# Kernel tuning notes

Hardware: AMD Instinct MI355X
Metric: run time of the kernel (lower is better)

## Reference

```python
import jax, jax.numpy as jnp
import numpy as np

B, S, V, E, H, C = 64, 256, 50000, 512, 512, 20


def _lstm_dir(x, w_ih, w_hh, b_ih, b_hh):
    # x: [B,S,E]; PyTorch gate order i,f,g,o; returns hidden seq [B,S,H]
    h_dim = w_hh.shape[1]
    xproj = jnp.einsum('bse,ge->bsg', x, w_ih) + b_ih  # [B,S,4H]
    h0 = jnp.zeros((x.shape[0], h_dim), x.dtype)

    def step(carry, xt):
        h, c = carry
        g = xt + h @ w_hh.T + b_hh
        i, f, gg, o = jnp.split(g, 4, axis=-1)
        c = jax.nn.sigmoid(f) * c + jax.nn.sigmoid(i) * jnp.tanh(gg)
        h = jax.nn.sigmoid(o) * jnp.tanh(c)
        return (h, c), h

    _, hs = jax.lax.scan(step, (h0, h0), jnp.swapaxes(xproj, 0, 1))
    return jnp.swapaxes(hs, 0, 1)  # [B,S,H]


def setup_inputs() -> dict:
    key = jax.random.key(0)
    ks = jax.random.split(key, 16)
    sc = lambda fan: 1.0 / np.sqrt(fan)
    return {
        'x': jax.random.randint(ks[0], (B, S), 0, V),
        'embed': jax.random.normal(ks[1], (V, E), jnp.float32),
        'w_ih_f': jax.random.normal(ks[2], (4 * H, E), jnp.float32) * sc(E),
        'w_hh_f': jax.random.normal(ks[3], (4 * H, H), jnp.float32) * sc(H),
        'b_ih_f': jax.random.normal(ks[4], (4 * H,), jnp.float32) * sc(H),
        'b_hh_f': jax.random.normal(ks[5], (4 * H,), jnp.float32) * sc(H),
        'w_ih_b': jax.random.normal(ks[6], (4 * H, E), jnp.float32) * sc(E),
        'w_hh_b': jax.random.normal(ks[7], (4 * H, H), jnp.float32) * sc(H),
        'b_ih_b': jax.random.normal(ks[8], (4 * H,), jnp.float32) * sc(H),
        'b_hh_b': jax.random.normal(ks[9], (4 * H,), jnp.float32) * sc(H),
        'myw': jax.random.normal(ks[10], (2 * H, 1), jnp.float32),
        'lin1_w': jax.random.normal(ks[11], (H, 2 * H), jnp.float32) * sc(2 * H),
        'lin1_b': jax.random.normal(ks[12], (H,), jnp.float32) * sc(2 * H),
        'lin2_w': jax.random.normal(ks[13], (C, H), jnp.float32) * sc(H),
        'lin2_b': jax.random.normal(ks[14], (C,), jnp.float32) * sc(H),
    }


def reference(x, embed, w_ih_f, w_hh_f, b_ih_f, b_hh_f,
              w_ih_b, w_hh_b, b_ih_b, b_hh_b,
              myw, lin1_w, lin1_b, lin2_w, lin2_b):
    emb = embed[x]                                   # [B,S,E] (dropout=eval no-op)
    h_f = _lstm_dir(emb, w_ih_f, w_hh_f, b_ih_f, b_hh_f)
    h_b = _lstm_dir(emb[:, ::-1], w_ih_b, w_hh_b, b_ih_b, b_hh_b)[:, ::-1]
    out = jnp.concatenate([h_f, h_b], axis=-1)       # [B,S,2H]
    # additive-ish attention: weights = exp(tanh(h . w)), normalized by row sum
    p = jnp.exp(jnp.tanh(jnp.einsum('bsd,d->bs', out, myw[:, 0])))  # [B,S]
    denom = jax.lax.stop_gradient(p.sum(axis=1, keepdims=True))     # .data in torch
    pooled = jnp.einsum('bs,bsd->bd', p / denom, out)               # [B,2H]
    h1 = pooled @ lin1_w.T + lin1_b
    return h1 @ lin2_w.T + lin2_b                     # [B,C]
```

## Files before the change

kernel.cpp:

```cpp
#include <hip/hip_runtime.h>

typedef _Float16 f16;
typedef _Float16 half8 __attribute__((ext_vector_type(8)));
typedef float floatx4 __attribute__((ext_vector_type(4)));
typedef unsigned long long u64;
typedef unsigned int u32;
typedef unsigned int u32v4 __attribute__((ext_vector_type(4)));

#define NB 64
#define NS 256
#define NE 512
#define NH 512
#define NG 2048
#define NN 4096

#define HB_B 40
#define HB_KT 320

#define OFF_XP     0
#define OFF_EMB    134217728
#define OFF_WCAT   150994944
#define OFF_WHH    155189248
#define OFF_HSEQ   159383552
#define OFF_BIAS   193200128
#define OFF_HEXT   OFF_EMB

__device__ __forceinline__ void cbar() {
  asm volatile("" ::: "memory");
}
__device__ __forceinline__ float fast_tanh(float x) {
  float e = __expf(2.f * x);
  return 1.f - 2.f / (1.f + e);
}
__device__ __forceinline__ u64 sysld(const u64* p) {
  return __hip_atomic_load(p, __ATOMIC_RELAXED, __HIP_MEMORY_SCOPE_SYSTEM);
}
__device__ __forceinline__ void glds16(const void* g, void* l) {
  __builtin_amdgcn_global_load_lds(
      (const __attribute__((address_space(1))) void*)g,
      (__attribute__((address_space(3))) void*)(__typeof__((__attribute__((address_space(3))) void*)0))(unsigned long)(l),
      16, 0, 0);
}

__global__ void k_prep(float* bias,
                       const float* bihf, const float* bhhf,
                       const float* bihb, const float* bhhb) {
  int id = blockIdx.x * 256 + threadIdx.x;
  bias[id] = (id < 2048) ? (bihf[id] + bhhf[id]) : (bihb[id - 2048] + bhhb[id - 2048]);
}

__global__ void k_zero(uint4* p) {
  uint4 z; z.x = 0; z.y = 0; z.z = 0; z.w = 0;
  p[blockIdx.x * 256 + threadIdx.x] = z;
}

__global__ void k_embed(const int* __restrict__ x, const float* __restrict__ embed,
                        f16* __restrict__ emb_h) {
  int gid = blockIdx.x * 256 + threadIdx.x;
  size_t base = (size_t)gid * 8;
  int r = (int)(base >> 9);
  int e = (int)(base & 511);
  int xi = x[r];
  const float4* src = (const float4*)(embed + (size_t)xi * 512 + e);
  float4 a = src[0], b = src[1];
  half8 h;
  h[0] = (f16)a.x; h[1] = (f16)a.y; h[2] = (f16)a.z; h[3] = (f16)a.w;
  h[4] = (f16)b.x; h[5] = (f16)b.y; h[6] = (f16)b.z; h[7] = (f16)b.w;
  *(half8*)(emb_h + base) = h;
}

__global__ void k_wcast(const float* __restrict__ wihf, const float* __restrict__ wihb,
                        const float* __restrict__ whhf, const float* __restrict__ whhb,
                        f16* __restrict__ w_cat, f16* __restrict__ whh) {
  int gid = blockIdx.x * 256 + threadIdx.x;
  size_t i8 = (size_t)gid * 8;
  const float* src;
  f16* dst;
  if (i8 < 2097152) {
    size_t n = i8 >> 9, k = i8 & 511;
    src = (n < 2048 ? wihf + n * 512 : wihb + (n - 2048) * 512) + k;
    dst = w_cat + i8;
  } else {
    size_t i2 = i8 - 2097152;
    int dir = (int)(i2 >> 20);
    size_t rk = i2 & 1048575;
    src = (dir ? whhb : whhf) + rk;
    dst = whh + i2;
  }
  float4 a = *(const float4*)src, b = *(const float4*)(src + 4);
  half8 h;
  h[0] = (f16)a.x; h[1] = (f16)a.y; h[2] = (f16)a.z; h[3] = (f16)a.w;
  h[4] = (f16)b.x; h[5] = (f16)b.y; h[6] = (f16)b.z; h[7] = (f16)b.w;
  *(half8*)dst = h;
}

__global__ __launch_bounds__(256) void k_gemm(const f16* __restrict__ A,
                                              const f16* __restrict__ Bw,
                                              const float* __restrict__ bias,
                                              f16* __restrict__ xp) {
  __shared__ __align__(16) f16 As[128 * 32];
  __shared__ __align__(16) f16 Bs[128 * 32];
  const int t = threadIdx.x;
  const int m0 = blockIdx.x * 128;
  const int n0 = blockIdx.y * 128;
  const int w = t >> 6, l = t & 63;
  const int wm = w >> 1, wn = w & 1;
  const int l15 = l & 15, q8 = (l >> 4) * 8;

  floatx4 acc[4][4];
#pragma unroll
  for (int mi = 0; mi < 4; mi++)
#pragma unroll
    for (int ni = 0; ni < 4; ni++) {
      acc[mi][ni][0] = 0.f; acc[mi][ni][1] = 0.f;
      acc[mi][ni][2] = 0.f; acc[mi][ni][3] = 0.f;
    }

  for (int kt = 0; kt < 16; kt++) {
#pragma unroll
    for (int i = 0; i < 2; i++) {
      int c = t + 256 * i;
      int row = c >> 2, kc = (c & 3) * 8;
      glds16(A + (size_t)(m0 + row) * 512 + kt * 32 + kc, &As[(64 * w + 256 * i) * 8]);
      glds16(Bw + (size_t)(n0 + row) * 512 + kt * 32 + kc, &Bs[(64 * w + 256 * i) * 8]);
    }
    asm volatile("s_waitcnt vmcnt(0)" ::: "memory");
    __syncthreads();
    half8 af[4], bf[4];
#pragma unroll
    for (int mi = 0; mi < 4; mi++)
      af[mi] = *(const half8*)&As[(wm * 64 + mi * 16 + l15) * 32 + q8];
#pragma unroll
    for (int ni = 0; ni < 4; ni++)
      bf[ni] = *(const half8*)&Bs[(wn * 64 + ni * 16 + l15) * 32 + q8];
#pragma unroll
    for (int mi = 0; mi < 4; mi++)
#pragma unroll
      for (int ni = 0; ni < 4; ni++)
        acc[mi][ni] = __builtin_amdgcn_mfma_f32_16x16x32_f16(af[mi], bf[ni], acc[mi][ni], 0, 0, 0);
    __syncthreads();
  }

#pragma unroll
  for (int ni = 0; ni < 4; ni++) {
    int ng = n0 + wn * 64 + ni * 16 + l15;
    float bv = bias[ng];
#pragma unroll
    for (int mi = 0; mi < 4; mi++) {
      int mg = m0 + wm * 64 + mi * 16 + (l >> 4) * 4;
#pragma unroll
      for (int r = 0; r < 4; r++)
        xp[(size_t)(mg + r) * 4096 + ng] = (f16)(acc[mi][ni][r] + bv);
    }
  }
}

__global__ __launch_bounds__(256) void k_rec(const f16* __restrict__ whh,
                                             const f16* __restrict__ xp,
                                             u32* __restrict__ h_ext,
                                             f16* __restrict__ h_seq) {
  const int blk = blockIdx.x;
  const int dir = blk & 1;
  const int bg  = (blk >> 1) & 7;
  const int jg  = blk >> 4;
  const int t = threadIdx.x;
  const int w = t >> 6, l = t & 63;
  const int l15 = l & 15, q = l >> 4;
  const int lb = l & 7;

  half8 fa[2][16];
  {
#pragma unroll
    for (int mi = 0; mi < 2; mi++) {
      const int gate = 2 * mi + (l15 >> 3);
      const f16* wb = whh + ((size_t)dir * 2048 + gate * 512 + jg * 32 + w * 8 + (l15 & 7)) * 512;
#pragma unroll
      for (int kt = 0; kt < 16; kt++)
        fa[mi][kt] = *(const half8*)(wb + kt * 32 + q * 8);
    }
  }

  __shared__ __align__(16) f16 hbuf[2][16 * HB_KT];
  __shared__ float zw[4][32][18];
  float creg = 0.f;

  const int cb = l >> 3, cu = l & 7;

  const size_t xrow = ((size_t)(8 * bg + lb) * 256);
  const int xc0 = dir * 2048 + (q >> 1) * 512 + jg * 32 + w * 8 + (q & 1) * 4;
  const int xc1 = xc0 + 1024;

  const int slab_rd_base = (dir * 8 + bg) * 4096;
  const int cl_dst0 = (t >> 4) * HB_KT + (t & 3) * 2 * HB_B + ((t >> 2) & 3) * 8;
  const int pub_idx = (jg * 4 + w) * 64 + l;
  const size_t hs_cbase = (size_t)((dir * 16 + jg) * 4 + w) * 256 * 512 + bg * 64 + l;

#pragma unroll 1
  for (int st = 0; st < NS; st++) {
    const int s = dir ? (255 - st) : st;
    const int p = st & 1;

    uint2 xv0 = *(const uint2*)(xp + (xrow + s) * NN + xc0);
    uint2 xv1 = *(const uint2*)(xp + (xrow + s) * NN + xc1);
    cbar();

    {
      const u32* slab32 = h_ext + (p * 16 * 4096) + slab_rd_base;
      const u64* sp = (const u64*)(slab32 + t * 16);
      const u64 tmask = 0xffff0000ffff0000ull;
      const u64 texp = ((u64)(u32)st << 16) | ((u64)(u32)st << 48);
      if (st) __builtin_amdgcn_s_sleep(8);
      while ((sysld(sp + 7) & tmask) != texp) __builtin_amdgcn_s_sleep(1);
      u64 w0, w1, w2, w3, w4, w5, w6, w7;
      while (true) {
        w0 = sysld(sp + 0); w1 = sysld(sp + 1); w2 = sysld(sp + 2); w3 = sysld(sp + 3);
        w4 = sysld(sp + 4); w5 = sysld(sp + 5); w6 = sysld(sp + 6); w7 = sysld(sp + 7);
        u64 ax = w0 & w1 & w2 & w3 & w4 & w5 & w6 & w7;
        u64 ox = w0 | w1 | w2 | w3 | w4 | w5 | w6 | w7;
        if (((ax & tmask) == texp) & ((ox & tmask) == texp)) break;
        __builtin_amdgcn_s_sleep(1);
      }
      u32v4 d0, d1;
      d0[0] = (u32)(w0 & 0xffffu) | ((u32)((w0 >> 32) & 0xffffu) << 16);
      d0[1] = (u32)(w1 & 0xffffu) | ((u32)((w1 >> 32) & 0xffffu) << 16);
      d0[2] = (u32)(w2 & 0xffffu) | ((u32)((w2 >> 32) & 0xffffu) << 16);
      d0[3] = (u32)(w3 & 0xffffu) | ((u32)((w3 >> 32) & 0xffffu) << 16);
      d1[0] = (u32)(w4 & 0xffffu) | ((u32)((w4 >> 32) & 0xffffu) << 16);
      d1[1] = (u32)(w5 & 0xffffu) | ((u32)((w5 >> 32) & 0xffffu) << 16);
      d1[2] = (u32)(w6 & 0xffffu) | ((u32)((w6 >> 32) & 0xffffu) << 16);
      d1[3] = (u32)(w7 & 0xffffu) | ((u32)((w7 >> 32) & 0xffffu) << 16);
      *(u32v4*)&hbuf[p][cl_dst0 + 0]    = d0;
      *(u32v4*)&hbuf[p][cl_dst0 + HB_B] = d1;
    }
    __syncthreads();

    floatx4 a0e, a0o, a1e, a1o;
    a0e[0]=0.f;a0e[1]=0.f;a0e[2]=0.f;a0e[3]=0.f;
    a0o[0]=0.f;a0o[1]=0.f;a0o[2]=0.f;a0o[3]=0.f;
    a1e[0]=0.f;a1e[1]=0.f;a1e[2]=0.f;a1e[3]=0.f;
    a1o[0]=0.f;a1o[1]=0.f;a1o[2]=0.f;a1o[3]=0.f;
#pragma unroll
    for (int kt = 0; kt < 16; kt += 2) {
      half8 bf0 = *(const half8*)&hbuf[p][kt * HB_KT + lb * HB_B + q * 8];
      half8 bf1 = *(const half8*)&hbuf[p][(kt + 1) * HB_KT + lb * HB_B + q * 8];
      a0e = __builtin_amdgcn_mfma_f32_16x16x32_f16(fa[0][kt], bf0, a0e, 0, 0, 0);
      a1e = __builtin_amdgcn_mfma_f32_16x16x32_f16(fa[1][kt], bf0, a1e, 0, 0, 0);
      a0o = __builtin_amdgcn_mfma_f32_16x16x32_f16(fa[0][kt + 1], bf1, a0o, 0, 0, 0);
      a1o = __builtin_amdgcn_mfma_f32_16x16x32_f16(fa[1][kt + 1], bf1, a1o, 0, 0, 0);
    }
    floatx4 acc0 = a0e + a0o;
    floatx4 acc1 = a1e + a1o;

    {
      const f16* x0 = (const f16*)&xv0;
      const f16* x1 = (const f16*)&xv1;
#pragma unroll
      for (int r = 0; r < 4; r++) {
        zw[w][q * 4 + r][l15]      = acc0[r] + (float)x0[r];
        zw[w][16 + q * 4 + r][l15] = acc1[r] + (float)x1[r];
      }
    }
    cbar();
    __builtin_amdgcn_wave_barrier();
    asm volatile("s_waitcnt lgkmcnt(0)" ::: "memory");
    __builtin_amdgcn_sched_barrier(0);

    {
      float iv = zw[w][cu][cb];
      float fv = zw[w][8 + cu][cb];
      float gv = zw[w][16 + cu][cb];
      float ov = zw[w][24 + cu][cb];
      float ig = 1.f / (1.f + __expf(-iv));
      float fg = 1.f / (1.f + __expf(-fv));
      float og = 1.f / (1.f + __expf(-ov));
      creg = fg * creg + ig * fast_tanh(gv);
      f16 hh = (f16)(og * fast_tanh(creg));
      unsigned short hb = __builtin_bit_cast(unsigned short, hh);
      u32 word = (u32)hb | ((u32)(st + 1) << 16);
      u32* wslab = h_ext + (((st + 1) & 1) * 16 * 4096) + slab_rd_base;
      __hip_atomic_store(wslab + pub_idx, word, __ATOMIC_RELAXED,
                         __HIP_MEMORY_SCOPE_SYSTEM);
      h_seq[hs_cbase + (size_t)s * 512] = hh;
    }
  }
}

__global__ __launch_bounds__(256) void k_attn(const f16* __restrict__ h_seq,
                                              const float* __restrict__ myw,
                                              const float* __restrict__ l1w,
                                              const float* __restrict__ l1b,
                                              const float* __restrict__ l2w,
                                              const float* __restrict__ l2b,
                                              float* __restrict__ out) {
  const int b = blockIdx.x;
  const int t = threadIdx.x;
  const int w = t >> 6, l = t & 63;
  float mw[16];
#pragma unroll
  for (int i = 0; i < 16; i += 4) {
    float4 v = *(const float4*)(myw + l * 16 + i);
    mw[i] = v.x; mw[i + 1] = v.y; mw[i + 2] = v.z; mw[i + 3] = v.w;
  }
  float pool[16];
#pragma unroll
  for (int i = 0; i < 16; i++) pool[i] = 0.f;
  float psum = 0.f;

  for (int s = w; s < NS; s += 4) {
    const f16* hp0 = h_seq + ((size_t)(2 * l) * 256 + s) * 512 + b * 8;
    const f16* hp1 = h_seq + ((size_t)(2 * l + 1) * 256 + s) * 512 + b * 8;
    half8 h0 = *(const half8*)hp0;
    half8 h1 = *(const half8*)hp1;
    float hv[16];
#pragma unroll
    for (int i = 0; i < 8; i++) { hv[i] = (float)h0[i]; hv[8 + i] = (float)h1[i]; }
    float d = 0.f;
#pragma unroll
    for (int i = 0; i < 16; i++) d += hv[i] * mw[i];
#pragma unroll
    for (int off = 32; off > 0; off >>= 1) d += __shfl_xor(d, off);
    float p = __expf(tanhf(d));
    psum += p;
#pragma unroll
    for (int i = 0; i < 16; i++) pool[i] += p * hv[i];
  }

  __shared__ float zb[4][1024];
  __shared__ float ps[4];
  __shared__ float pooled[1024];
  __shared__ float h1s[512];
#pragma unroll
  for (int i = 0; i < 16; i++) zb[w][l * 16 + i] = pool[i];
  if (l == 0) ps[w] = psum;
  __syncthreads();
  float denom = ps[0] + ps[1] + ps[2] + ps[3];
  for (int d0 = t; d0 < 1024; d0 += 256)
    pooled[d0] = (zb[0][d0] + zb[1][d0] + zb[2][d0] + zb[3][d0]) / denom;
  __syncthreads();
  for (int r = t; r < 512; r += 256) {
    const float* wr = l1w + (size_t)r * 1024;
    float a = l1b[r];
    for (int k = 0; k < 1024; k += 4) {
      float4 wv = *(const float4*)(wr + k);
      a += wv.x * pooled[k] + wv.y * pooled[k + 1] + wv.z * pooled[k + 2] + wv.w * pooled[k + 3];
    }
    h1s[r] = a;
  }
  __syncthreads();
  if (t < 20) {
    const float* wr = l2w + t * 512;
    float a = l2b[t];
    for (int k = 0; k < 512; k++) a += h1s[k] * wr[k];
    out[b * 20 + t] = a;
  }
}

extern "C" void kernel_launch(void* const* d_in, const int* in_sizes, int n_in,
                              void* d_out, int out_size, void* d_ws, size_t ws_size,
                              hipStream_t stream) {
  (void)in_sizes; (void)n_in; (void)out_size; (void)ws_size;
  const int*   x     = (const int*)d_in[0];
  const float* embed = (const float*)d_in[1];
  const float* wihf  = (const float*)d_in[2];
  const float* whhf  = (const float*)d_in[3];
  const float* bihf  = (const float*)d_in[4];
  const float* bhhf  = (const float*)d_in[5];
  const float* wihb  = (const float*)d_in[6];
  const float* whhb  = (const float*)d_in[7];
  const float* bihb  = (const float*)d_in[8];
  const float* bhhb  = (const float*)d_in[9];
  const float* myw   = (const float*)d_in[10];
  const float* l1w   = (const float*)d_in[11];
  const float* l1b   = (const float*)d_in[12];
  const float* l2w   = (const float*)d_in[13];
  const float* l2b   = (const float*)d_in[14];

  char* ws = (char*)d_ws;
  f16*   xp    = (f16*)(ws + OFF_XP);
  f16*   emb_h = (f16*)(ws + OFF_EMB);
  f16*   w_cat = (f16*)(ws + OFF_WCAT);
  f16*   whh   = (f16*)(ws + OFF_WHH);
  f16*   h_seq = (f16*)(ws + OFF_HSEQ);
  u32*   h_ext = (u32*)(ws + OFF_HEXT);
  float* bias  = (float*)(ws + OFF_BIAS);
  float* out   = (float*)d_out;

  k_prep<<<16, 256, 0, stream>>>(bias, bihf, bhhf, bihb, bhhb);
  k_embed<<<4096, 256, 0, stream>>>(x, embed, emb_h);
  k_wcast<<<2048, 256, 0, stream>>>(wihf, wihb, whhf, whhb, w_cat, whh);
  k_gemm<<<dim3(128, 32), 256, 0, stream>>>(emb_h, w_cat, bias, xp);
  k_zero<<<128, 256, 0, stream>>>((uint4*)(ws + OFF_HEXT));
  k_rec<<<256, 256, 0, stream>>>(whh, xp, h_ext, h_seq);
  k_attn<<<64, 256, 0, stream>>>(h_seq, myw, l1w, l1b, l2w, l2b, out);
}
```

Measured before the change: 1.082 ms.

## Process two batch groups per recurrent block and halve the grid

Each recurrent block now handles two batch groups (bg and bg+4) in turn within every timestep. The register-resident W_hh fragments are reused across both groups, and the launch drops from 256 to 128 blocks. The intent is to cut the number of blocks polling the global handoff slabs and to let one group's work proceed while the other's hidden state is still arriving. The fixed s_sleep before polling is also removed. In exchange, each block does twice the serial work per step, with two block-wide barriers per step, which may lengthen the recurrence critical path.

```diff
diff --git a/kernel.cpp b/kernel.cpp
--- a/kernel.cpp
+++ b/kernel.cpp
@@ -161,8 +161,8 @@
                                              f16* __restrict__ h_seq) {
   const int blk = blockIdx.x;
   const int dir = blk & 1;
-  const int bg  = (blk >> 1) & 7;
-  const int jg  = blk >> 4;
+  const int bgp = (blk >> 1) & 3;
+  const int jg  = blk >> 3;
   const int t = threadIdx.x;
   const int w = t >> 6, l = t & 63;
   const int l15 = l & 15, q = l >> 4;
@@ -180,107 +180,121 @@
     }
   }
 
-  __shared__ __align__(16) f16 hbuf[2][16 * HB_KT];
+  __shared__ __align__(16) f16 hbuf[2][2][16 * HB_KT];
   __shared__ float zw[4][32][18];
-  float creg = 0.f;
+  float creg0 = 0.f, creg1 = 0.f;
 
   const int cb = l >> 3, cu = l & 7;
 
-  const size_t xrow = ((size_t)(8 * bg + lb) * 256);
   const int xc0 = dir * 2048 + (q >> 1) * 512 + jg * 32 + w * 8 + (q & 1) * 4;
   const int xc1 = xc0 + 1024;
 
-  const int slab_rd_base = (dir * 8 + bg) * 4096;
+  const int bgA = bgp, bgB = bgp + 4;
+  const size_t xrowA = ((size_t)(8 * bgA + lb) * 256);
+  const size_t xrowB = ((size_t)(8 * bgB + lb) * 256);
+  const int rdA = (dir * 8 + bgA) * 4096;
+  const int rdB = (dir * 8 + bgB) * 4096;
   const int cl_dst0 = (t >> 4) * HB_KT + (t & 3) * 2 * HB_B + ((t >> 2) & 3) * 8;
   const int pub_idx = (jg * 4 + w) * 64 + l;
-  const size_t hs_cbase = (size_t)((dir * 16 + jg) * 4 + w) * 256 * 512 + bg * 64 + l;
+  const size_t hs_chunk = (size_t)((dir * 16 + jg) * 4 + w) * 256 * 512;
+  const size_t hsA = hs_chunk + bgA * 64 + l;
+  const size_t hsB = hs_chunk + bgB * 64 + l;
+
+  const u64 tmask = 0xffff0000ffff0000ull;
 
 #pragma unroll 1
   for (int st = 0; st < NS; st++) {
     const int s = dir ? (255 - st) : st;
     const int p = st & 1;
-
-    uint2 xv0 = *(const uint2*)(xp + (xrow + s) * NN + xc0);
-    uint2 xv1 = *(const uint2*)(xp + (xrow + s) * NN + xc1);
+    const u64 texp = ((u64)(u32)st << 16) | ((u64)(u32)st << 48);
+
+    uint2 xa0 = *(const uint2*)(xp + (xrowA + s) * NN + xc0);
+    uint2 xa1 = *(const uint2*)(xp + (xrowA + s) * NN + xc1);
+    uint2 xb0 = *(const uint2*)(xp + (xrowB + s) * NN + xc0);
+    uint2 xb1 = *(const uint2*)(xp + (xrowB + s) * NN + xc1);
     cbar();
 
-    {
-      const u32* slab32 = h_ext + (p * 16 * 4096) + slab_rd_base;
-      const u64* sp = (const u64*)(slab32 + t * 16);
-      const u64 tmask = 0xffff0000ffff0000ull;
-      const u64 texp = ((u64)(u32)st << 16) | ((u64)(u32)st << 48);
-      if (st) __builtin_amdgcn_s_sleep(8);
-      while ((sysld(sp + 7) & tmask) != texp) __builtin_amdgcn_s_sleep(1);
-      u64 w0, w1, w2, w3, w4, w5, w6, w7;
-      while (true) {
-        w0 = sysld(sp + 0); w1 = sysld(sp + 1); w2 = sysld(sp + 2); w3 = sysld(sp + 3);
-        w4 = sysld(sp + 4); w5 = sysld(sp + 5); w6 = sysld(sp + 6); w7 = sysld(sp + 7);
-        u64 ax = w0 & w1 & w2 & w3 & w4 & w5 & w6 & w7;
-        u64 ox = w0 | w1 | w2 | w3 | w4 | w5 | w6 | w7;
-        if (((ax & tmask) == texp) & ((ox & tmask) == texp)) break;
-        __builtin_amdgcn_s_sleep(1);
+#pragma unroll
+    for (int c = 0; c < 2; c++) {
+      const int rdb = c ? rdB : rdA;
+      f16* hb = &hbuf[c][p][0];
+
+      {
+        const u32* slab32 = h_ext + (p * 16 * 4096) + rdb;
+        const u64* sp = (const u64*)(slab32 + t * 16);
+        u64 w0, w1, w2, w3, w4, w5, w6, w7;
+        while (true) {
+          w0 = sysld(sp + 0); w1 = sysld(sp + 1); w2 = sysld(sp + 2); w3 = sysld(sp + 3);
+          w4 = sysld(sp + 4); w5 = sysld(sp + 5); w6 = sysld(sp + 6); w7 = sysld(sp + 7);
+          u64 ax = w0 & w1 & w2 & w3 & w4 & w5 & w6 & w7;
+          u64 ox = w0 | w1 | w2 | w3 | w4 | w5 | w6 | w7;
+          if (((ax & tmask) == texp) & ((ox & tmask) == texp)) break;
+          __builtin_amdgcn_s_sleep(1);
+        }
+        u32v4 d0, d1;
+        d0[0] = (u32)(w0 & 0xffffu) | ((u32)((w0 >> 32) & 0xffffu) << 16);
+        d0[1] = (u32)(w1 & 0xffffu) | ((u32)((w1 >> 32) & 0xffffu) << 16);
+        d0[2] = (u32)(w2 & 0xffffu) | ((u32)((w2 >> 32) & 0xffffu) << 16);
+        d0[3] = (u32)(w3 & 0xffffu) | ((u32)((w3 >> 32) & 0xffffu) << 16);
+        d1[0] = (u32)(w4 & 0xffffu) | ((u32)((w4 >> 32) & 0xffffu) << 16);
+        d1[1] = (u32)(w5 & 0xffffu) | ((u32)((w5 >> 32) & 0xffffu) << 16);
+        d1[2] = (u32)(w6 & 0xffffu) | ((u32)((w6 >> 32) & 0xffffu) << 16);
+        d1[3] = (u32)(w7 & 0xffffu) | ((u32)((w7 >> 32) & 0xffffu) << 16);
+        *(u32v4*)&hb[cl_dst0 + 0]    = d0;
+        *(u32v4*)&hb[cl_dst0 + HB_B] = d1;
       }
-      u32v4 d0, d1;
-      d0[0] = (u32)(w0 & 0xffffu) | ((u32)((w0 >> 32) & 0xffffu) << 16);
-      d0[1] = (u32)(w1 & 0xffffu) | ((u32)((w1 >> 32) & 0xffffu) << 16);
-      d0[2] = (u32)(w2 & 0xffffu) | ((u32)((w2 >> 32) & 0xffffu) << 16);
-      d0[3] = (u32)(w3 & 0xffffu) | ((u32)((w3 >> 32) & 0xffffu) << 16);
-      d1[0] = (u32)(w4 & 0xffffu) | ((u32)((w4 >> 32) & 0xffffu) << 16);
-      d1[1] = (u32)(w5 & 0xffffu) | ((u32)((w5 >> 32) & 0xffffu) << 16);
-      d1[2] = (u32)(w6 & 0xffffu) | ((u32)((w6 >> 32) & 0xffffu) << 16);
-      d1[3] = (u32)(w7 & 0xffffu) | ((u32)((w7 >> 32) & 0xffffu) << 16);
-      *(u32v4*)&hbuf[p][cl_dst0 + 0]    = d0;
-      *(u32v4*)&hbuf[p][cl_dst0 + HB_B] = d1;
-    }
-    __syncthreads();
-
-    floatx4 a0e, a0o, a1e, a1o;
-    a0e[0]=0.f;a0e[1]=0.f;a0e[2]=0.f;a0e[3]=0.f;
-    a0o[0]=0.f;a0o[1]=0.f;a0o[2]=0.f;a0o[3]=0.f;
-    a1e[0]=0.f;a1e[1]=0.f;a1e[2]=0.f;a1e[3]=0.f;
-    a1o[0]=0.f;a1o[1]=0.f;a1o[2]=0.f;a1o[3]=0.f;
-#pragma unroll
-    for (int kt = 0; kt < 16; kt += 2) {
-      half8 bf0 = *(const half8*)&hbuf[p][kt * HB_KT + lb * HB_B + q * 8];
-      half8 bf1 = *(const half8*)&hbuf[p][(kt + 1) * HB_KT + lb * HB_B + q * 8];
-      a0e = __builtin_amdgcn_mfma_f32_16x16x32_f16(fa[0][kt], bf0, a0e, 0, 0, 0);
-      a1e = __builtin_amdgcn_mfma_f32_16x16x32_f16(fa[1][kt], bf0, a1e, 0, 0, 0);
-      a0o = __builtin_amdgcn_mfma_f32_16x16x32_f16(fa[0][kt + 1], bf1, a0o, 0, 0, 0);
-      a1o = __builtin_amdgcn_mfma_f32_16x16x32_f16(fa[1][kt + 1], bf1, a1o, 0, 0, 0);
-    }
-    floatx4 acc0 = a0e + a0o;
-    floatx4 acc1 = a1e + a1o;
-
-    {
-      const f16* x0 = (const f16*)&xv0;
-      const f16* x1 = (const f16*)&xv1;
-#pragma unroll
-      for (int r = 0; r < 4; r++) {
-        zw[w][q * 4 + r][l15]      = acc0[r] + (float)x0[r];
-        zw[w][16 + q * 4 + r][l15] = acc1[r] + (float)x1[r];
+      __syncthreads();
+
+      floatx4 a0e, a0o, a1e, a1o;
+      a0e[0]=0.f;a0e[1]=0.f;a0e[2]=0.f;a0e[3]=0.f;
+      a0o[0]=0.f;a0o[1]=0.f;a0o[2]=0.f;a0o[3]=0.f;
+      a1e[0]=0.f;a1e[1]=0.f;a1e[2]=0.f;a1e[3]=0.f;
+      a1o[0]=0.f;a1o[1]=0.f;a1o[2]=0.f;a1o[3]=0.f;
+#pragma unroll
+      for (int kt = 0; kt < 16; kt += 2) {
+        half8 bf0 = *(const half8*)&hb[kt * HB_KT + lb * HB_B + q * 8];
+        half8 bf1 = *(const half8*)&hb[(kt + 1) * HB_KT + lb * HB_B + q * 8];
+        a0e = __builtin_amdgcn_mfma_f32_16x16x32_f16(fa[0][kt], bf0, a0e, 0, 0, 0);
+        a1e = __builtin_amdgcn_mfma_f32_16x16x32_f16(fa[1][kt], bf0, a1e, 0, 0, 0);
+        a0o = __builtin_amdgcn_mfma_f32_16x16x32_f16(fa[0][kt + 1], bf1, a0o, 0, 0, 0);
+        a1o = __builtin_amdgcn_mfma_f32_16x16x32_f16(fa[1][kt + 1], bf1, a1o, 0, 0, 0);
       }
-    }
-    cbar();
-    __builtin_amdgcn_wave_barrier();
-    asm volatile("s_waitcnt lgkmcnt(0)" ::: "memory");
-    __builtin_amdgcn_sched_barrier(0);
-
-    {
-      float iv = zw[w][cu][cb];
-      float fv = zw[w][8 + cu][cb];
-      float gv = zw[w][16 + cu][cb];
-      float ov = zw[w][24 + cu][cb];
-      float ig = 1.f / (1.f + __expf(-iv));
-      float fg = 1.f / (1.f + __expf(-fv));
-      float og = 1.f / (1.f + __expf(-ov));
-      creg = fg * creg + ig * fast_tanh(gv);
-      f16 hh = (f16)(og * fast_tanh(creg));
-      unsigned short hb = __builtin_bit_cast(unsigned short, hh);
-      u32 word = (u32)hb | ((u32)(st + 1) << 16);
-      u32* wslab = h_ext + (((st + 1) & 1) * 16 * 4096) + slab_rd_base;
-      __hip_atomic_store(wslab + pub_idx, word, __ATOMIC_RELAXED,
-                         __HIP_MEMORY_SCOPE_SYSTEM);
-      h_seq[hs_cbase + (size_t)s * 512] = hh;
+      floatx4 acc0 = a0e + a0o;
+      floatx4 acc1 = a1e + a1o;
+
+      {
+        const f16* x0 = (const f16*)(c ? &xb0 : &xa0);
+        const f16* x1 = (const f16*)(c ? &xb1 : &xa1);
+#pragma unroll
+        for (int r = 0; r < 4; r++) {
+          zw[w][q * 4 + r][l15]      = acc0[r] + (float)x0[r];
+          zw[w][16 + q * 4 + r][l15] = acc1[r] + (float)x1[r];
+        }
+      }
+      cbar();
+      __builtin_amdgcn_wave_barrier();
+      asm volatile("s_waitcnt lgkmcnt(0)" ::: "memory");
+      __builtin_amdgcn_sched_barrier(0);
+
+      {
+        float iv = zw[w][cu][cb];
+        float fv = zw[w][8 + cu][cb];
+        float gv = zw[w][16 + cu][cb];
+        float ov = zw[w][24 + cu][cb];
+        float ig = 1.f / (1.f + __expf(-iv));
+        float fg = 1.f / (1.f + __expf(-fv));
+        float og = 1.f / (1.f + __expf(-ov));
+        float cr = c ? creg1 : creg0;
+        cr = fg * cr + ig * fast_tanh(gv);
+        if (c) creg1 = cr; else creg0 = cr;
+        f16 hh = (f16)(og * fast_tanh(cr));
+        unsigned short hb16 = __builtin_bit_cast(unsigned short, hh);
+        u32 word = (u32)hb16 | ((u32)(st + 1) << 16);
+        u32* wslab = h_ext + (((st + 1) & 1) * 16 * 4096) + rdb;
+        __hip_atomic_store(wslab + pub_idx, word, __ATOMIC_RELAXED,
+                           __HIP_MEMORY_SCOPE_SYSTEM);
+        h_seq[(c ? hsB : hsA) + (size_t)s * 512] = hh;
+      }
     }
   }
 }
@@ -390,6 +404,6 @@
   k_wcast<<<2048, 256, 0, stream>>>(wihf, wihb, whhf, whhb, w_cat, whh);
   k_gemm<<<dim3(128, 32), 256, 0, stream>>>(emb_h, w_cat, bias, xp);
   k_zero<<<128, 256, 0, stream>>>((uint4*)(ws + OFF_HEXT));
-  k_rec<<<256, 256, 0, stream>>>(whh, xp, h_ext, h_seq);
+  k_rec<<<128, 256, 0, stream>>>(whh, xp, h_ext, h_seq);
   k_attn<<<64, 256, 0, stream>>>(h_seq, myw, l1w, l1b, l2w, l2b, out);
 }
```

Result: slower. 1.435 ms (+32.6%).
